# Kernel tuning notes

Hardware: AMD Instinct MI355X
Metric: run time of the kernel (lower is better)

## Reference

```python
import jax, jax.numpy as jnp
import numpy as np

B, S, H, NH, HD = 2, 2048, 4096, 32, 128
NEG = jnp.finfo(jnp.float32).min


def rotate_half(x):
    x1, x2 = x[..., : x.shape[-1] // 2], x[..., x.shape[-1] // 2 :]
    return jnp.concatenate((-x2, x1), axis=-1)


def setup_inputs() -> dict:
    key = jax.random.key(0)
    ks = jax.random.split(key, 7)
    return {
        "hidden_states": jax.random.normal(ks[0], (B, S, H), jnp.float32),
        "cos": jax.random.uniform(ks[1], (1, 1, S, HD), jnp.float32),
        "sin": jax.random.uniform(ks[2], (1, 1, S, HD), jnp.float32),
        "Wq": jax.random.normal(ks[3], (H, H), jnp.float32) * 0.02,
        "Wk": jax.random.normal(ks[4], (HD, H), jnp.float32) * 0.02,
        "Wv": jax.random.normal(ks[5], (HD, H), jnp.float32) * 0.02,
        "Wd": jax.random.normal(ks[6], (H, H), jnp.float32) * 0.02,
    }


def reference(hidden_states, cos, sin, Wq, Wk, Wv, Wd):
    b, s, _ = hidden_states.shape
    q = (hidden_states @ Wq.T).reshape(b, s, NH, HD).transpose(0, 2, 1, 3)  # [B,NH,S,HD]
    k = (hidden_states @ Wk.T)[:, None, :, :]  # [B,1,S,HD] (multi-query)
    v = (hidden_states @ Wv.T)[:, None, :, :]
    # inline RoPE
    q = q * cos + rotate_half(q) * sin
    k = k * cos + rotate_half(k) * sin
    scale = 1.0 / jnp.sqrt(jnp.float32(HD))
    scores = jnp.einsum("bhqd,bhkd->bhqk", q, k) * scale
    # causal mask: additive finfo.min above diagonal
    causal = jnp.tril(jnp.ones((s, s), jnp.bool_))
    scores = scores + jnp.where(causal, 0.0, NEG)
    attn = jax.nn.softmax(scores, axis=-1)
    out = jnp.einsum("bhqk,bhkd->bhqd", attn, v)  # [B,NH,S,HD]
    out = out.transpose(0, 2, 1, 3).reshape(b, s, NH * HD)
    return out @ Wd.T
```

## Files before the change

### kernel.cpp

```cpp
#include <hip/hip_runtime.h>
#include <hip/hip_bf16.h>
#include <math.h>

constexpr int Bc  = 2;
constexpr int Sc  = 2048;
constexpr int Hc  = 4096;
constexpr int NHc = 32;
constexpr int HDc = 128;

typedef __attribute__((ext_vector_type(8))) __bf16 bf16x8;
typedef __attribute__((ext_vector_type(4))) __bf16 bf16x4;
typedef __attribute__((ext_vector_type(4))) float  f32x4;

#if defined(__has_builtin)
#if __has_builtin(__builtin_amdgcn_global_load_lds)
#define HAS_GLL 1
#endif
#endif
#ifndef HAS_GLL
#define HAS_GLL 0
#endif

__device__ __forceinline__ float fast_exp2(float x) {
#if defined(__has_builtin)
#if __has_builtin(__builtin_amdgcn_exp2f)
    return __builtin_amdgcn_exp2f(x);
#else
    return exp2f(x);
#endif
#else
    return exp2f(x);
#endif
}

#define CFENCE asm volatile("" ::: "memory")
#define BARRIER do { CFENCE; __builtin_amdgcn_s_barrier(); CFENCE; } while (0)
#define WAITVM(n) asm volatile("s_waitcnt vmcnt(" #n ")" ::: "memory")

__device__ __forceinline__ void gll16(const __bf16* g, __bf16* lds_base, int lane) {
#if HAS_GLL
    __builtin_amdgcn_global_load_lds((const __attribute__((address_space(1))) void*)g,
                                     (__attribute__((address_space(3))) void*)lds_base,
                                     16, 0, 0);
#else
    *(int4*)(lds_base + lane * 8) = *(const int4*)g;
#endif
}

__global__ void cvt_f32_bf16(const float* __restrict__ in, __bf16* __restrict__ out, int n) {
    int i = (blockIdx.x * blockDim.x + threadIdx.x) * 4;
    if (i >= n) return;
    const float4 v = *(const float4*)(in + i);
    bf16x4 o;
    o[0] = (__bf16)v.x; o[1] = (__bf16)v.y; o[2] = (__bf16)v.z; o[3] = (__bf16)v.w;
    *(bf16x4*)(out + i) = o;
}

__global__ void build_wkv(const float* __restrict__ Wk, const float* __restrict__ Wv,
                          __bf16* __restrict__ out) {
    int i = (blockIdx.x * blockDim.x + threadIdx.x) * 4;
    if (i >= 256 * Hc) return;
    int row = i >> 12;
    int col = i & (Hc - 1);
    const float* src = (row < HDc) ? (Wk + (long)row * Hc + col)
                                   : (Wv + (long)(row - HDc) * Hc + col);
    const float4 v = *(const float4*)src;
    bf16x4 o;
    o[0] = (__bf16)v.x; o[1] = (__bf16)v.y; o[2] = (__bf16)v.z; o[3] = (__bf16)v.w;
    *(bf16x4*)(out + i) = o;
}

template <typename OUT>
__global__ __launch_bounds__(512, 2)
void gemm256(const __bf16* __restrict__ A, const __bf16* __restrict__ B,
             OUT* __restrict__ C, int M, int N, int K) {
    __shared__ __bf16 As[2][256 * 64];
    __shared__ __bf16 Bs[2][256 * 64];

    const int tid  = threadIdx.x;
    const int wave = tid >> 6, lane = tid & 63;
    const int lrow = lane & 15, quad = lane >> 4;
    const int wm = wave >> 2, wn = wave & 3;

    const int nwg = gridDim.x * gridDim.y;
    const int bid = blockIdx.y * gridDim.x + blockIdx.x;
    const int wg  = (bid & 7) * (nwg >> 3) + (bid >> 3);
    const int m0  = (wg / gridDim.x) * 256;
    const int n0  = (wg % gridDim.x) * 256;

    f32x4 acc[8][4] = {};

    int srow[4][2], sbase[4][2];
    const int rp   = lane >> 3;
    const int scol = ((lane & 7) ^ rp) << 3;
#pragma unroll
    for (int it = 0; it < 2; ++it) {
        const int c   = wave * 2 + it;
        const int rb0 = (c < 8) ? c * 8 : 128 + (c - 8) * 8;
        const int rb1 = (c >> 2) * 64 + (c & 3) * 8;
        srow[0][it] = rb0 + rp;       sbase[0][it] = rb0 * 64;
        srow[1][it] = rb1 + rp;       sbase[1][it] = rb1 * 64;
        srow[2][it] = rb1 + 32 + rp;  sbase[2][it] = (rb1 + 32) * 64;
        srow[3][it] = rb0 + 64 + rp;  sbase[3][it] = (rb0 + 64) * 64;
    }
    const __bf16* Ab = A + (long)m0 * K;
    const __bf16* Bb = B + (long)n0 * K;

    auto stageg = [&](int g, int bu, long k0) {
        const __bf16* gb = (g == 0 || g == 3) ? Ab : Bb;
        __bf16* lb = (g == 0 || g == 3) ? &As[bu][0] : &Bs[bu][0];
#pragma unroll
        for (int it = 0; it < 2; ++it)
            gll16(gb + (long)srow[g][it] * K + k0 + scol, lb + sbase[g][it], lane);
    };

    const int fc0  = ((quad ^ (lrow & 7)) << 3);
    const int fc1  = (((4 | quad) ^ (lrow & 7)) << 3);
    const int arow = wm * 128 + lrow;
    const int brow = wn * 64 + lrow;

    const int nk = K >> 6;
    stageg(0, 0, 0); stageg(1, 0, 0); stageg(2, 0, 0); stageg(3, 0, 0);
    WAITVM(4);
    BARRIER;

    for (int kt = 0; kt < nk; ++kt) {
        const int bu = kt & 1;
        const bool more = (kt + 1 < nk);
        const long k1 = (long)(kt + 1) * 64;
        bf16x8 af[2][4], bv0[2][2], bv1[2][2];

#pragma unroll
        for (int i2 = 0; i2 < 4; ++i2) {
            af[0][i2] = *(const bf16x8*)&As[bu][(arow + i2 * 16) * 64 + fc0];
            af[1][i2] = *(const bf16x8*)&As[bu][(arow + i2 * 16) * 64 + fc1];
        }
#pragma unroll
        for (int j2 = 0; j2 < 2; ++j2) {
            bv0[0][j2] = *(const bf16x8*)&Bs[bu][(brow + j2 * 16) * 64 + fc0];
            bv0[1][j2] = *(const bf16x8*)&Bs[bu][(brow + j2 * 16) * 64 + fc1];
        }
        if (more) { stageg(0, bu ^ 1, k1); WAITVM(4); } else { WAITVM(0); }
        BARRIER;
        __builtin_amdgcn_s_setprio(1);
#pragma unroll
        for (int c = 0; c < 2; ++c)
#pragma unroll
            for (int i2 = 0; i2 < 4; ++i2)
#pragma unroll
                for (int j2 = 0; j2 < 2; ++j2)
                    acc[i2][j2] = __builtin_amdgcn_mfma_f32_16x16x32_bf16(
                        af[c][i2], bv0[c][j2], acc[i2][j2], 0, 0, 0);
        __builtin_amdgcn_s_setprio(0);
        BARRIER;

#pragma unroll
        for (int j2 = 0; j2 < 2; ++j2) {
            bv1[0][j2] = *(const bf16x8*)&Bs[bu][(brow + 32 + j2 * 16) * 64 + fc0];
            bv1[1][j2] = *(const bf16x8*)&Bs[bu][(brow + 32 + j2 * 16) * 64 + fc1];
        }
        if (more) { stageg(1, bu ^ 1, k1); WAITVM(4); } else { WAITVM(0); }
        BARRIER;
        __builtin_amdgcn_s_setprio(1);
#pragma unroll
        for (int c = 0; c < 2; ++c)
#pragma unroll
            for (int i2 = 0; i2 < 4; ++i2)
#pragma unroll
                for (int j2 = 0; j2 < 2; ++j2)
                    acc[i2][2 + j2] = __builtin_amdgcn_mfma_f32_16x16x32_bf16(
                        af[c][i2], bv1[c][j2], acc[i2][2 + j2], 0, 0, 0);
        __builtin_amdgcn_s_setprio(0);
        BARRIER;

#pragma unroll
        for (int i2 = 0; i2 < 4; ++i2) {
            af[0][i2] = *(const bf16x8*)&As[bu][(arow + 64 + i2 * 16) * 64 + fc0];
            af[1][i2] = *(const bf16x8*)&As[bu][(arow + 64 + i2 * 16) * 64 + fc1];
        }
        if (more) { stageg(2, bu ^ 1, k1); WAITVM(4); } else { WAITVM(0); }
        BARRIER;
        __builtin_amdgcn_s_setprio(1);
#pragma unroll
        for (int c = 0; c < 2; ++c)
#pragma unroll
            for (int i2 = 0; i2 < 4; ++i2)
#pragma unroll
                for (int j2 = 0; j2 < 2; ++j2)
                    acc[4 + i2][j2] = __builtin_amdgcn_mfma_f32_16x16x32_bf16(
                        af[c][i2], bv0[c][j2], acc[4 + i2][j2], 0, 0, 0);
        __builtin_amdgcn_s_setprio(0);
        BARRIER;

        if (more) { stageg(3, bu ^ 1, k1); WAITVM(4); } else { WAITVM(0); }
        BARRIER;
        __builtin_amdgcn_s_setprio(1);
#pragma unroll
        for (int c = 0; c < 2; ++c)
#pragma unroll
            for (int i2 = 0; i2 < 4; ++i2)
#pragma unroll
                for (int j2 = 0; j2 < 2; ++j2)
                    acc[4 + i2][2 + j2] = __builtin_amdgcn_mfma_f32_16x16x32_bf16(
                        af[c][i2], bv1[c][j2], acc[4 + i2][2 + j2], 0, 0, 0);
        __builtin_amdgcn_s_setprio(0);
        BARRIER;
    }

#pragma unroll
    for (int i = 0; i < 8; ++i) {
        const int row = m0 + wm * 128 + i * 16 + quad * 4;
#pragma unroll
        for (int j = 0; j < 4; ++j) {
            const int col = n0 + wn * 64 + j * 16 + lrow;
            OUT* cp = C + (long)row * N + col;
#pragma unroll
            for (int r = 0; r < 4; ++r) cp[(long)r * N] = (OUT)acc[i][j][r];
        }
    }
}

template <typename OUT>
__global__ __launch_bounds__(256)
void gemm_bt64(const __bf16* __restrict__ A, const __bf16* __restrict__ B,
               OUT* __restrict__ C, int M, int N, int K) {
    __shared__ __bf16 As[64][64];
    __shared__ __bf16 Bs[64][64];

    const int tid  = threadIdx.x;
    const int wave = tid >> 6, lane = tid & 63;
    const int lrow = lane & 15, quad = lane >> 4;
    const int m0   = blockIdx.y * 64;
    const int n0   = blockIdx.x * 64;
    const int wr   = (wave >> 1) * 32;
    const int wc   = (wave & 1) * 32;

    f32x4 acc[2][2] = {};

    int srow[2], scol[2];
#pragma unroll
    for (int it = 0; it < 2; ++it) {
        int e = (wave * 2 + it) * 1024 + lane * 16;
        int r = e >> 7;
        int cb = (e >> 4) & 7;
        srow[it] = r;
        scol[it] = ((cb ^ (r & 7)) * 8);
    }
    const __bf16* Ab = A + (long)m0 * K;
    const __bf16* Bb = B + (long)n0 * K;

    const int fcol0 = ((quad ^ (lrow & 7)) << 3);
    const int fcol1 = (((4 | quad) ^ (lrow & 7)) << 3);

    const int nk = K >> 6;
    for (int kt = 0; kt < nk; ++kt) {
        const long k0 = (long)kt * 64;
        __syncthreads();
#pragma unroll
        for (int it = 0; it < 2; ++it)
            gll16(Ab + (long)srow[it] * K + k0 + scol[it], &As[0][0] + (wave * 2 + it) * 512, lane);
#pragma unroll
        for (int it = 0; it < 2; ++it)
            gll16(Bb + (long)srow[it] * K + k0 + scol[it], &Bs[0][0] + (wave * 2 + it) * 512, lane);
        __syncthreads();

#pragma unroll
        for (int c = 0; c < 2; ++c) {
            const int fc = c ? fcol1 : fcol0;
            bf16x8 af[2], bfv[2];
#pragma unroll
            for (int i = 0; i < 2; ++i) af[i]  = *(const bf16x8*)&As[wr + i * 16 + lrow][fc];
#pragma unroll
            for (int j = 0; j < 2; ++j) bfv[j] = *(const bf16x8*)&Bs[wc + j * 16 + lrow][fc];
#pragma unroll
            for (int i = 0; i < 2; ++i)
#pragma unroll
                for (int j = 0; j < 2; ++j)
                    acc[i][j] = __builtin_amdgcn_mfma_f32_16x16x32_bf16(af[i], bfv[j], acc[i][j], 0, 0, 0);
        }
    }

#pragma unroll
    for (int i = 0; i < 2; ++i) {
        const int row = m0 + wr + i * 16 + quad * 4;
#pragma unroll
        for (int j = 0; j < 2; ++j) {
            const int col = n0 + wc + j * 16 + lrow;
            OUT* cp = C + (long)row * N + col;
#pragma unroll
            for (int r = 0; r < 4; ++r) cp[(long)r * N] = (OUT)acc[i][j][r];
        }
    }
}

__global__ void rope_k(__bf16* __restrict__ KV, const float* __restrict__ cosb,
                       const float* __restrict__ sinb) {
    int gid  = blockIdx.x * blockDim.x + threadIdx.x;
    int row  = gid >> 3;
    int dblk = (gid & 7) * 8;
    int s    = row & (Sc - 1);
    __bf16* p = KV + (long)row * 256;
    const float* cp = cosb + s * HDc;
    const float* sp = sinb + s * HDc;
    bf16x8 lo = *(bf16x8*)(p + dblk);
    bf16x8 hi = *(bf16x8*)(p + dblk + 64);
    bf16x8 olo, ohi;
#pragma unroll
    for (int j = 0; j < 8; ++j) {
        float ql = (float)lo[j], qh = (float)hi[j];
        float cl = cp[dblk + j],      sl = sp[dblk + j];
        float ch = cp[dblk + 64 + j], sh = sp[dblk + 64 + j];
        olo[j] = (__bf16)(ql * cl - qh * sl);
        ohi[j] = (__bf16)(qh * ch + ql * sh);
    }
    *(bf16x8*)(p + dblk)      = olo;
    *(bf16x8*)(p + dblk + 64) = ohi;
}

__global__ void vtrans(const __bf16* __restrict__ KV, __bf16* __restrict__ Vt) {
    __shared__ __bf16 T[128][72];
    const int tid = threadIdx.x;
    const int s0  = (blockIdx.x & (Sc / 64 - 1)) * 64;
    const int b   = blockIdx.x / (Sc / 64);
#pragma unroll
    for (int i = 0; i < 4; ++i) {
        int e = i * 256 + tid;
        int s = e >> 4, dc = (e & 15) * 8;
        bf16x8 v = *(const bf16x8*)(KV + (long)(b * Sc + s0 + s) * 256 + 128 + dc);
#pragma unroll
        for (int j = 0; j < 8; ++j) T[dc + j][s] = v[j];
    }
    __syncthreads();
#pragma unroll
    for (int i = 0; i < 4; ++i) {
        int e = i * 256 + tid;
        int d = e >> 3, sc8 = (e & 7) * 8;
        bf16x8 v;
#pragma unroll
        for (int j = 0; j < 8; ++j) v[j] = T[d][sc8 + j];
        *(bf16x8*)(Vt + (long)(b * HDc + d) * Sc + s0 + sc8) = v;
    }
}

__global__ __launch_bounds__(256, 2)
void attn(const __bf16* __restrict__ Q,
          const __bf16* __restrict__ KV,
          const __bf16* __restrict__ Vt,
          const float* __restrict__ cosb,
          const float* __restrict__ sinb,
          __bf16* __restrict__ O) {
    const int qt   = (gridDim.x - 1) - blockIdx.x;
    const int bh   = blockIdx.y;
    const int b    = bh >> 5, h = bh & 31;
    const int tid  = threadIdx.x;
    const int wave = tid >> 6, lane = tid & 63;
    const int lrow = lane & 15, quad = lane >> 4;

    __shared__ __bf16 Ks[2][64][128];
    __shared__ __bf16 Vs[2][128][64];
    __shared__ __bf16 Ps[4][16][72];

    bf16x8 vone;
#pragma unroll
    for (int j = 0; j < 8; ++j) vone[j] = (__bf16)1.0f;

    const int q0 = qt * 128 + wave * 32;

    const float qscale = 0.08838834764831845f * 1.4426950408889634f;
    bf16x8 aq[2][4];
#pragma unroll
    for (int qq = 0; qq < 2; ++qq) {
        const int s = q0 + qq * 16 + lrow;
        const __bf16* qp = Q + (long)(b * Sc + s) * Hc + h * HDc + quad * 8;
        const float* cp = cosb + s * HDc + quad * 8;
        const float* sp = sinb + s * HDc + quad * 8;
        bf16x8 raw[4];
#pragma unroll
        for (int c = 0; c < 4; ++c) raw[c] = *(const bf16x8*)(qp + c * 32);
#pragma unroll
        for (int c = 0; c < 2; ++c) {
#pragma unroll
            for (int j = 0; j < 8; ++j) {
                const int d = c * 32 + j;
                float ql = (float)raw[c][j], qh = (float)raw[c + 2][j];
                float cl = cp[d],      sl = sp[d];
                float ch = cp[d + 64], sh = sp[d + 64];
                aq[qq][c][j]     = (__bf16)((ql * cl - qh * sl) * qscale);
                aq[qq][c + 2][j] = (__bf16)((qh * ch + ql * sh) * qscale);
            }
        }
    }

    f32x4 o[2][8] = {};
    f32x4 lac[2] = {};
    float mst[2][4];
#pragma unroll
    for (int qq = 0; qq < 2; ++qq)
#pragma unroll
        for (int r = 0; r < 4; ++r) mst[qq][r] = -3.0e38f;

    const __bf16* kvb = KV + (long)b * Sc * 256;
    const __bf16* vtb = Vt + (long)b * HDc * Sc;
    int krow[4], kcol[4], vrow[4], vcol[4];
#pragma unroll
    for (int it = 0; it < 4; ++it) {
        int e = (wave * 4 + it) * 1024 + lane * 16;
        int rk = e >> 8, cbk = (e >> 4) & 15;
        krow[it] = rk; kcol[it] = ((cbk ^ (rk & 15)) * 8);
        int rv = e >> 7, cbv = (e >> 4) & 7;
        vrow[it] = rv; vcol[it] = ((cbv ^ (rv & 7)) * 8);
    }

    auto stage = [&](int kt, int bu) {
#pragma unroll
        for (int it = 0; it < 4; ++it) {
            gll16(kvb + (long)(kt * 64 + krow[it]) * 256 + kcol[it],
                  &Ks[bu][0][0] + (wave * 4 + it) * 512, lane);
            gll16(vtb + (long)vrow[it] * Sc + kt * 64 + vcol[it],
                  &Vs[bu][0][0] + (wave * 4 + it) * 512, lane);
        }
    };

    const int nt = 2 * qt + 2;
    stage(0, 0);

    for (int kt = 0; kt < nt; ++kt) {
        __syncthreads();
        if (kt + 1 < nt) stage(kt + 1, (kt + 1) & 1);
        const int bu = kt & 1;

        f32x4 sc[2][4] = {};
        __builtin_amdgcn_s_setprio(1);
#pragma unroll
        for (int ct = 0; ct < 4; ++ct) {
#pragma unroll
            for (int c = 0; c < 4; ++c) {
                bf16x8 bk = *(const bf16x8*)&Ks[bu][ct * 16 + lrow][(((c << 2) | quad) ^ lrow) << 3];
                sc[0][ct] = __builtin_amdgcn_mfma_f32_16x16x32_bf16(aq[0][c], bk, sc[0][ct], 0, 0, 0);
                sc[1][ct] = __builtin_amdgcn_mfma_f32_16x16x32_bf16(aq[1][c], bk, sc[1][ct], 0, 0, 0);
            }
        }
        __builtin_amdgcn_s_setprio(0);

        bf16x8 ap[2][2];
#pragma unroll
        for (int qq = 0; qq < 2; ++qq) {
            if (kt * 64 + 63 > q0 + qq * 16) {
#pragma unroll
                for (int ct = 0; ct < 4; ++ct) {
                    int kv = kt * 64 + ct * 16 + lrow;
#pragma unroll
                    for (int r = 0; r < 4; ++r) {
                        int qr = q0 + qq * 16 + quad * 4 + r;
                        if (kv > qr) sc[qq][ct][r] = -3.0e38f;
                    }
                }
            }

            float lmax[4];
#pragma unroll
            for (int r = 0; r < 4; ++r)
                lmax[r] = fmaxf(fmaxf(sc[qq][0][r], sc[qq][1][r]),
                                fmaxf(sc[qq][2][r], sc[qq][3][r]));
            const bool near_ok = (lmax[0] <= mst[qq][0] + 8.0f) &&
                                 (lmax[1] <= mst[qq][1] + 8.0f) &&
                                 (lmax[2] <= mst[qq][2] + 8.0f) &&
                                 (lmax[3] <= mst[qq][3] + 8.0f);
            if (!__all(near_ok)) {
                float alf[4];
#pragma unroll
                for (int r = 0; r < 4; ++r) {
                    float mx = lmax[r];
#pragma unroll
                    for (int off = 1; off < 16; off <<= 1) mx = fmaxf(mx, __shfl_xor(mx, off, 64));
                    float mnew = fmaxf(mst[qq][r], mx);
                    alf[r]     = fast_exp2(mst[qq][r] - mnew);
                    mst[qq][r] = mnew;
                }
#pragma unroll
                for (int dt = 0; dt < 8; ++dt)
#pragma unroll
                    for (int r = 0; r < 4; ++r) o[qq][dt][r] *= alf[r];
#pragma unroll
                for (int r = 0; r < 4; ++r) lac[qq][r] *= alf[r];
            }
#pragma unroll
            for (int ct = 0; ct < 4; ++ct)
#pragma unroll
                for (int r = 0; r < 4; ++r)
                    sc[qq][ct][r] = fast_exp2(sc[qq][ct][r] - mst[qq][r]);

#pragma unroll
            for (int ct = 0; ct < 4; ++ct)
#pragma unroll
                for (int r = 0; r < 4; ++r)
                    Ps[wave][quad * 4 + r][ct * 16 + lrow] = (__bf16)sc[qq][ct][r];
#pragma unroll
            for (int ks = 0; ks < 2; ++ks)
                ap[qq][ks] = *(const bf16x8*)&Ps[wave][lrow][ks * 32 + quad * 8];
        }

        __builtin_amdgcn_s_setprio(1);
#pragma unroll
        for (int dt = 0; dt < 8; ++dt) {
#pragma unroll
            for (int ks = 0; ks < 2; ++ks) {
                bf16x8 bv = *(const bf16x8*)&Vs[bu][dt * 16 + lrow]
                                [(((ks << 2) | quad) ^ (lrow & 7)) << 3];
#pragma unroll
                for (int qq = 0; qq < 2; ++qq)
                    o[qq][dt] = __builtin_amdgcn_mfma_f32_16x16x32_bf16(ap[qq][ks], bv, o[qq][dt], 0, 0, 0);
            }
        }
#pragma unroll
        for (int ks = 0; ks < 2; ++ks) {
#pragma unroll
            for (int qq = 0; qq < 2; ++qq)
                lac[qq] = __builtin_amdgcn_mfma_f32_16x16x32_bf16(ap[qq][ks], vone, lac[qq], 0, 0, 0);
        }
        __builtin_amdgcn_s_setprio(0);
    }

#pragma unroll
    for (int qq = 0; qq < 2; ++qq)
#pragma unroll
        for (int r = 0; r < 4; ++r) {
            float inv = 1.f / lac[qq][r];
            int qr = q0 + qq * 16 + quad * 4 + r;
            __bf16* op = O + (long)(b * Sc + qr) * Hc + h * HDc;
#pragma unroll
            for (int dt = 0; dt < 8; ++dt) op[dt * 16 + lrow] = (__bf16)(o[qq][dt][r] * inv);
        }
}

extern "C" void kernel_launch(void* const* d_in, const int* in_sizes, int n_in,
                              void* d_out, int out_size, void* d_ws, size_t ws_size,
                              hipStream_t stream) {
    const float* hs   = (const float*)d_in[0];
    const float* cosb = (const float*)d_in[1];
    const float* sinb = (const float*)d_in[2];
    const float* Wq   = (const float*)d_in[3];
    const float* Wk   = (const float*)d_in[4];
    const float* Wv   = (const float*)d_in[5];
    const float* Wd   = (const float*)d_in[6];
    float* out = (float*)d_out;

    char* ws = (char*)d_ws;
    const long SZ_HS  = (long)Bc * Sc * Hc * 2;
    const long SZ_W   = (long)Hc * Hc * 2;
    const long SZ_KV  = (long)Bc * Sc * 256 * 2;
    __bf16* hs16  = (__bf16*)(ws);
    __bf16* wq16  = (__bf16*)(ws + SZ_HS);
    __bf16* wkv16 = (__bf16*)(ws + SZ_HS + SZ_W);
    __bf16* q16   = (__bf16*)(ws + SZ_HS + SZ_W + SZ_KV);
    __bf16* kv16  = (__bf16*)(ws + SZ_HS + SZ_W + SZ_KV + SZ_HS);
    __bf16* vt16  = (__bf16*)(ws + SZ_HS + SZ_W + SZ_KV + SZ_HS + SZ_KV);
    __bf16* att16 = hs16;
    __bf16* wd16  = wq16;

    const int nHS = Bc * Sc * Hc;
    const int nW  = Hc * Hc;

    cvt_f32_bf16<<<nHS / 1024, 256, 0, stream>>>(hs, hs16, nHS);
    cvt_f32_bf16<<<nW / 1024, 256, 0, stream>>>(Wq, wq16, nW);
    build_wkv<<<(256 * Hc) / 1024, 256, 0, stream>>>(Wk, Wv, wkv16);

    gemm256<__bf16><<<dim3(Hc / 256, (Bc * Sc) / 256), 512, 0, stream>>>(
        hs16, wq16, q16, Bc * Sc, Hc, Hc);
    gemm_bt64<__bf16><<<dim3(256 / 64, (Bc * Sc) / 64), 256, 0, stream>>>(
        hs16, wkv16, kv16, Bc * Sc, 256, Hc);

    cvt_f32_bf16<<<nW / 1024, 256, 0, stream>>>(Wd, wd16, nW);

    rope_k<<<(Bc * Sc * 8) / 256, 256, 0, stream>>>(kv16, cosb, sinb);
    vtrans<<<Bc * (Sc / 64), 256, 0, stream>>>(kv16, vt16);

    attn<<<dim3(Sc / 128, Bc * NHc), 256, 0, stream>>>(q16, kv16, vt16, cosb, sinb, att16);

    gemm256<float><<<dim3(Hc / 256, (Bc * Sc) / 256), 512, 0, stream>>>(
        att16, wd16, out, Bc * Sc, Hc, Hc);
}
```

Before: 665.1 us.

## Double-buffer gemm_bt64 tiles; single-buffer attention K/V with split staging

The 64x64 GEMM now double-buffers its A/B shared tiles and prefetches the next k-tile while computing the current one, which drops one barrier per iteration. The attention kernel goes from double-buffered K/V shared memory to single buffers, and raises launch_bounds to 3 blocks per CU to get more occupancy. In attention, K for the next tile is loaded right after QK^T and V right after PV, with vmcnt waits and barriers between them. This adds barriers and exposes more load latency per block, in exchange for more resident blocks.

```diff
diff --git a/kernel.cpp b/kernel.cpp
--- a/kernel.cpp
+++ b/kernel.cpp
@@ -224,8 +224,8 @@
 __global__ __launch_bounds__(256)
 void gemm_bt64(const __bf16* __restrict__ A, const __bf16* __restrict__ B,
                OUT* __restrict__ C, int M, int N, int K) {
-    __shared__ __bf16 As[64][64];
-    __shared__ __bf16 Bs[64][64];
+    __shared__ __bf16 As[2][64][64];
+    __shared__ __bf16 Bs[2][64][64];
 
     const int tid  = threadIdx.x;
     const int wave = tid >> 6, lane = tid & 63;
@@ -249,29 +249,34 @@
     const __bf16* Ab = A + (long)m0 * K;
     const __bf16* Bb = B + (long)n0 * K;
 
+    auto stage = [&](int kt, int bu) {
+        const long k0 = (long)kt * 64;
+#pragma unroll
+        for (int it = 0; it < 2; ++it)
+            gll16(Ab + (long)srow[it] * K + k0 + scol[it], &As[bu][0][0] + (wave * 2 + it) * 512, lane);
+#pragma unroll
+        for (int it = 0; it < 2; ++it)
+            gll16(Bb + (long)srow[it] * K + k0 + scol[it], &Bs[bu][0][0] + (wave * 2 + it) * 512, lane);
+    };
+
     const int fcol0 = ((quad ^ (lrow & 7)) << 3);
     const int fcol1 = (((4 | quad) ^ (lrow & 7)) << 3);
 
     const int nk = K >> 6;
+    stage(0, 0);
     for (int kt = 0; kt < nk; ++kt) {
-        const long k0 = (long)kt * 64;
         __syncthreads();
-#pragma unroll
-        for (int it = 0; it < 2; ++it)
-            gll16(Ab + (long)srow[it] * K + k0 + scol[it], &As[0][0] + (wave * 2 + it) * 512, lane);
-#pragma unroll
-        for (int it = 0; it < 2; ++it)
-            gll16(Bb + (long)srow[it] * K + k0 + scol[it], &Bs[0][0] + (wave * 2 + it) * 512, lane);
-        __syncthreads();
+        if (kt + 1 < nk) stage(kt + 1, (kt + 1) & 1);
+        const int bu = kt & 1;
 
 #pragma unroll
         for (int c = 0; c < 2; ++c) {
             const int fc = c ? fcol1 : fcol0;
             bf16x8 af[2], bfv[2];
 #pragma unroll
-            for (int i = 0; i < 2; ++i) af[i]  = *(const bf16x8*)&As[wr + i * 16 + lrow][fc];
-#pragma unroll
-            for (int j = 0; j < 2; ++j) bfv[j] = *(const bf16x8*)&Bs[wc + j * 16 + lrow][fc];
+            for (int i = 0; i < 2; ++i) af[i]  = *(const bf16x8*)&As[bu][wr + i * 16 + lrow][fc];
+#pragma unroll
+            for (int j = 0; j < 2; ++j) bfv[j] = *(const bf16x8*)&Bs[bu][wc + j * 16 + lrow][fc];
 #pragma unroll
             for (int i = 0; i < 2; ++i)
 #pragma unroll
@@ -342,7 +347,7 @@
     }
 }
 
-__global__ __launch_bounds__(256, 2)
+__global__ __launch_bounds__(256, 3)
 void attn(const __bf16* __restrict__ Q,
           const __bf16* __restrict__ KV,
           const __bf16* __restrict__ Vt,
@@ -356,8 +361,8 @@
     const int wave = tid >> 6, lane = tid & 63;
     const int lrow = lane & 15, quad = lane >> 4;
 
-    __shared__ __bf16 Ks[2][64][128];
-    __shared__ __bf16 Vs[2][128][64];
+    __shared__ __bf16 Ks[64][128];
+    __shared__ __bf16 Vs[128][64];
     __shared__ __bf16 Ps[4][16][72];
 
     bf16x8 vone;
@@ -365,6 +370,34 @@
     for (int j = 0; j < 8; ++j) vone[j] = (__bf16)1.0f;
 
     const int q0 = qt * 128 + wave * 32;
+
+    const __bf16* kvb = KV + (long)b * Sc * 256;
+    const __bf16* vtb = Vt + (long)b * HDc * Sc;
+    int krow[4], kcol[4], vrow[4], vcol[4];
+#pragma unroll
+    for (int it = 0; it < 4; ++it) {
+        int e = (wave * 4 + it) * 1024 + lane * 16;
+        int rk = e >> 8, cbk = (e >> 4) & 15;
+        krow[it] = rk; kcol[it] = ((cbk ^ (rk & 15)) * 8);
+        int rv = e >> 7, cbv = (e >> 4) & 7;
+        vrow[it] = rv; vcol[it] = ((cbv ^ (rv & 7)) * 8);
+    }
+
+    auto stage_k = [&](int kt) {
+#pragma unroll
+        for (int it = 0; it < 4; ++it)
+            gll16(kvb + (long)(kt * 64 + krow[it]) * 256 + kcol[it],
+                  &Ks[0][0] + (wave * 4 + it) * 512, lane);
+    };
+    auto stage_v = [&](int kt) {
+#pragma unroll
+        for (int it = 0; it < 4; ++it)
+            gll16(vtb + (long)vrow[it] * Sc + kt * 64 + vcol[it],
+                  &Vs[0][0] + (wave * 4 + it) * 512, lane);
+    };
+
+    stage_k(0);
+    stage_v(0);
 
     const float qscale = 0.08838834764831845f * 1.4426950408889634f;
     bf16x8 aq[2][4];
@@ -399,35 +432,13 @@
 #pragma unroll
         for (int r = 0; r < 4; ++r) mst[qq][r] = -3.0e38f;
 
-    const __bf16* kvb = KV + (long)b * Sc * 256;
-    const __bf16* vtb = Vt + (long)b * HDc * Sc;
-    int krow[4], kcol[4], vrow[4], vcol[4];
-#pragma unroll
-    for (int it = 0; it < 4; ++it) {
-        int e = (wave * 4 + it) * 1024 + lane * 16;
-        int rk = e >> 8, cbk = (e >> 4) & 15;
-        krow[it] = rk; kcol[it] = ((cbk ^ (rk & 15)) * 8);
-        int rv = e >> 7, cbv = (e >> 4) & 7;
-        vrow[it] = rv; vcol[it] = ((cbv ^ (rv & 7)) * 8);
-    }
-
-    auto stage = [&](int kt, int bu) {
-#pragma unroll
-        for (int it = 0; it < 4; ++it) {
-            gll16(kvb + (long)(kt * 64 + krow[it]) * 256 + kcol[it],
-                  &Ks[bu][0][0] + (wave * 4 + it) * 512, lane);
-            gll16(vtb + (long)vrow[it] * Sc + kt * 64 + vcol[it],
-                  &Vs[bu][0][0] + (wave * 4 + it) * 512, lane);
-        }
-    };
-
     const int nt = 2 * qt + 2;
-    stage(0, 0);
 
     for (int kt = 0; kt < nt; ++kt) {
-        __syncthreads();
-        if (kt + 1 < nt) stage(kt + 1, (kt + 1) & 1);
-        const int bu = kt & 1;
+        const bool more = (kt + 1 < nt);
+
+        WAITVM(4);
+        BARRIER;
 
         f32x4 sc[2][4] = {};
         __builtin_amdgcn_s_setprio(1);
@@ -435,12 +446,15 @@
         for (int ct = 0; ct < 4; ++ct) {
 #pragma unroll
             for (int c = 0; c < 4; ++c) {
-                bf16x8 bk = *(const bf16x8*)&Ks[bu][ct * 16 + lrow][(((c << 2) | quad) ^ lrow) << 3];
+                bf16x8 bk = *(const bf16x8*)&Ks[ct * 16 + lrow][(((c << 2) | quad) ^ lrow) << 3];
                 sc[0][ct] = __builtin_amdgcn_mfma_f32_16x16x32_bf16(aq[0][c], bk, sc[0][ct], 0, 0, 0);
                 sc[1][ct] = __builtin_amdgcn_mfma_f32_16x16x32_bf16(aq[1][c], bk, sc[1][ct], 0, 0, 0);
             }
         }
         __builtin_amdgcn_s_setprio(0);
+
+        BARRIER;
+        if (more) stage_k(kt + 1);
 
         bf16x8 ap[2][2];
 #pragma unroll
@@ -500,12 +514,15 @@
                 ap[qq][ks] = *(const bf16x8*)&Ps[wave][lrow][ks * 32 + quad * 8];
         }
 
+        if (more) { WAITVM(4); } else { WAITVM(0); }
+        BARRIER;
+
         __builtin_amdgcn_s_setprio(1);
 #pragma unroll
         for (int dt = 0; dt < 8; ++dt) {
 #pragma unroll
             for (int ks = 0; ks < 2; ++ks) {
-                bf16x8 bv = *(const bf16x8*)&Vs[bu][dt * 16 + lrow]
+                bf16x8 bv = *(const bf16x8*)&Vs[dt * 16 + lrow]
                                 [(((ks << 2) | quad) ^ (lrow & 7)) << 3];
 #pragma unroll
                 for (int qq = 0; qq < 2; ++qq)
@@ -519,6 +536,9 @@
                 lac[qq] = __builtin_amdgcn_mfma_f32_16x16x32_bf16(ap[qq][ks], vone, lac[qq], 0, 0, 0);
         }
         __builtin_amdgcn_s_setprio(0);
+
+        BARRIER;
+        if (more) stage_v(kt + 1);
     }
 
 #pragma unroll
```

Measured after the change: 830.0 us. +24.8%, slower.
